# Kernel optimization log

Hardware: AMD Instinct MI355X
Metric: run time of the kernel (lower is better)

The kernel has to match this reference:

```python
import jax, jax.numpy as jnp
import numpy as np

NUM_NODES = 100000
EMB = 64
HID = 128
OUT = 64
N_EDGES = 1600000
N_LABEL = 200000


def setup_inputs() -> dict:
    key = jax.random.key(0)
    ks = jax.random.split(key, 8)
    return {
        "emb": jax.random.normal(ks[0], (NUM_NODES, EMB), jnp.float32) * 0.05,
        "w1l": jax.random.normal(ks[1], (HID, EMB), jnp.float32) * 0.05,
        "w1r": jax.random.normal(ks[2], (HID, EMB), jnp.float32) * 0.05,
        "b1": jnp.zeros((HID,), jnp.float32),
        "w2l": jax.random.normal(ks[3], (OUT, HID), jnp.float32) * 0.05,
        "w2r": jax.random.normal(ks[4], (OUT, HID), jnp.float32) * 0.05,
        "b2": jnp.zeros((OUT,), jnp.float32),
        "edge_index": jax.random.randint(ks[5], (2, N_EDGES), 0, NUM_NODES, jnp.int32),
        "edge_label_index": jax.random.randint(ks[6], (2, N_LABEL), 0, NUM_NODES, jnp.int32),
    }


def reference(emb, w1l, w1r, b1, w2l, w2r, b2, edge_index, edge_label_index):
    # PyG SAGEConv (aggr='mean'): out = mean_{j in N(i)} x_j @ W_l^T + b_l + x_i @ W_r^T
    n = emb.shape[0]
    src, dst = edge_index[0], edge_index[1]
    # in-degree per destination node, clamped to avoid div-by-zero (isolated nodes -> 0 agg)
    deg = jax.ops.segment_sum(jnp.ones(src.shape, emb.dtype), dst, num_segments=n)
    inv_deg = 1.0 / jnp.maximum(deg, 1.0)

    def sage(x, wl, wr, b):
        agg = jax.ops.segment_sum(x[src], dst, num_segments=n) * inv_deg[:, None]
        return agg @ wl.T + x @ wr.T + b

    h = jax.nn.relu(sage(emb, w1l, w1r, b1))  # dropout is identity in eval mode
    z = sage(h, w2l, w2r, b2)  # [N, OUT]
    # dot-product decode over candidate pairs
    return jnp.sum(z[edge_label_index[0]] * z[edge_label_index[1]], axis=-1)
```

## Files before the change

kernel.cpp:

```cpp
#include <hip/hip_runtime.h>

#define NN   100000
#define EMB  64
#define HID  128
#define OUTD 64
#define NE   1600000
#define NL   200000
#define NBUK 782
#define CAPT 2560

#define BIN_BLOCKS  160
#define TILE        10240
#define CEMB_BLOCKS 400
#define CW_BLOCKS   32

typedef __attribute__((ext_vector_type(4))) float f32x4;
typedef __attribute__((ext_vector_type(8))) short s16x8;
typedef __attribute__((ext_vector_type(4))) unsigned short us4;

__device__ __forceinline__ unsigned short f2bf(float f) {
    unsigned u = __float_as_uint(f);
    u += 0x7FFFu + ((u >> 16) & 1u);
    return (unsigned short)(u >> 16);
}
__device__ __forceinline__ float bf2f(unsigned short h) {
    return __uint_as_float(((unsigned)h) << 16);
}

__global__ void __launch_bounds__(512) prep_kernel(
        const int* __restrict__ src, const int* __restrict__ dst,
        int* __restrict__ gcur, int* __restrict__ tmp,
        const float* __restrict__ emb, unsigned short* __restrict__ embb,
        const float* __restrict__ w1l, const float* __restrict__ w1r,
        const float* __restrict__ w2l, const float* __restrict__ w2r,
        unsigned short* __restrict__ w1cat, unsigned short* __restrict__ w2cat) {
    const int bid = blockIdx.x;
    const int tid = threadIdx.x;

    if (bid < BIN_BLOCKS) {
        __shared__ int hist[NBUK];
        __shared__ int base[NBUK];
        const int t0  = bid * TILE;
        const int end = min(t0 + TILE, NE);

        for (int k = tid; k < NBUK; k += 512) hist[k] = 0;
        __syncthreads();

        for (int i = t0 + tid; i < end; i += 512)
            atomicAdd(&hist[__builtin_nontemporal_load(dst + i) >> 7], 1);
        __syncthreads();

        for (int k = tid; k < NBUK; k += 512) {
            int c = hist[k];
            base[k] = c ? atomicAdd(&gcur[k], c) : 0;
        }
        __syncthreads();

        for (int i = t0 + tid; i < end; i += 512) {
            int d = __builtin_nontemporal_load(dst + i);
            int s = __builtin_nontemporal_load(src + i);
            int b = d >> 7;
            int pos = atomicAdd(&base[b], 1);
            if (pos < CAPT) tmp[b * CAPT + pos] = ((d & 127) << 17) | s;
        }
    } else if (bid < BIN_BLOCKS + CEMB_BLOCKS) {
        for (int i = (bid - BIN_BLOCKS) * 512 + tid; i < NN * 16; i += CEMB_BLOCKS * 512) {
            float4 v = ((const float4*)emb)[i];
            us4 o;
            o.x = f2bf(v.x); o.y = f2bf(v.y); o.z = f2bf(v.z); o.w = f2bf(v.w);
            ((us4*)embb)[i] = o;
        }
    } else {
        int t = (bid - BIN_BLOCKS - CEMB_BLOCKS) * 512 + tid;
        if (t >= 128 * 128) return;
        int o = t >> 7, k = t & 127;
        w1cat[t] = f2bf(k < 64 ? w1l[o * 64 + k] : w1r[o * 64 + (k - 64)]);
        w2cat[t] = f2bf(o < 64 ? w2l[o * 128 + k] : w2r[(o - 64) * 128 + k]);
    }
}

template<bool L1>
__global__ void __launch_bounds__(512) agg_kernel(
        const int* __restrict__ gcur, const int* __restrict__ tmp,
        const unsigned short* __restrict__ xb,
        const float* __restrict__ hz, const float* __restrict__ bias,
        unsigned short* __restrict__ outb) {
    __shared__ int scnt[128];
    __shared__ int soff[128];
    __shared__ int scur[128];
    __shared__ int slist[CAPT];

    const int b    = blockIdx.x;
    const int tid  = threadIdx.x;
    const int lane = tid & 63;
    const int wv   = tid >> 6;

    if (tid < 128) scnt[tid] = 0;
    __syncthreads();

    const int cnt = min(gcur[b], CAPT);
    const int* tb = tmp + b * CAPT;

    for (int i = tid; i < cnt; i += 512)
        atomicAdd(&scnt[tb[i] >> 17], 1);
    __syncthreads();

    if (tid == 0) {
        int acc = 0;
        for (int r = 0; r < 128; ++r) {
            soff[r] = acc;
            scur[r] = acc;
            acc += scnt[r];
        }
    }
    __syncthreads();

    for (int i = tid; i < cnt; i += 512) {
        int p = tb[i];
        int pos = atomicAdd(&scur[p >> 17], 1);
        slist[pos] = p & 0x1FFFF;
    }
    __syncthreads();

    const float bb = L1 ? 0.f : bias[lane];

#define LDX(c) bf2f(xb[(size_t)(c) * 64 + lane])
    for (int r = wv; r < 128; r += 8) {
        const int node = b * 128 + r;
        if (node >= NN) continue;
        const int s = soff[r];
        const int d = scnt[r];
        float acc = 0.f;
        int j = 0;
        for (; j + 8 <= d; j += 8) {
            int c0 = slist[s + j + 0], c1 = slist[s + j + 1];
            int c2 = slist[s + j + 2], c3 = slist[s + j + 3];
            int c4 = slist[s + j + 4], c5 = slist[s + j + 5];
            int c6 = slist[s + j + 6], c7 = slist[s + j + 7];
            float v0 = LDX(c0), v1 = LDX(c1), v2 = LDX(c2), v3 = LDX(c3);
            float v4 = LDX(c4), v5 = LDX(c5), v6 = LDX(c6), v7 = LDX(c7);
            acc += ((v0 + v1) + (v2 + v3)) + ((v4 + v5) + (v6 + v7));
        }
        if (j + 4 <= d) {
            int c0 = slist[s + j + 0], c1 = slist[s + j + 1];
            int c2 = slist[s + j + 2], c3 = slist[s + j + 3];
            float v0 = LDX(c0), v1 = LDX(c1), v2 = LDX(c2), v3 = LDX(c3);
            acc += (v0 + v1) + (v2 + v3);
            j += 4;
        }
        for (; j < d; ++j) acc += LDX(slist[s + j]);

        const float inv = 1.0f / fmaxf((float)d, 1.0f);
        if (L1) {
            outb[(size_t)node * 64 + lane] = f2bf(acc * inv);
        } else {
            outb[(size_t)node * 64 + lane] =
                f2bf(acc * inv + hz[(size_t)node * 64 + lane] + bb);
        }
    }
#undef LDX
}

__global__ void __launch_bounds__(256) gemm_mfma_kernel(
        const unsigned short* __restrict__ aggb, const unsigned short* __restrict__ embb,
        const unsigned short* __restrict__ w1cat, const float* __restrict__ b1,
        const unsigned short* __restrict__ w2cat,
        unsigned short* __restrict__ p2b, float* __restrict__ hz) {
    __shared__ unsigned short h_lds[128 * 136];

    const int tid  = threadIdx.x;
    const int lane = tid & 63;
    const int w    = tid >> 6;
    const int l15  = lane & 15;
    const int lk   = lane >> 4;
    const int n_base = blockIdx.x * 128;
    const int mrow0  = w * 32;

    f32x4 acc[2][8];
#pragma unroll
    for (int mt = 0; mt < 2; ++mt)
#pragma unroll
        for (int nt = 0; nt < 8; ++nt) acc[mt][nt] = (f32x4)(0.f);

#pragma unroll
    for (int ks = 0; ks < 4; ++ks) {
        const int kc = ks * 32 + lk * 8;
        s16x8 a[2];
#pragma unroll
        for (int mt = 0; mt < 2; ++mt) {
            int n = n_base + mrow0 + mt * 16 + l15;
            s16x8 av = (s16x8)(short)0;
            if (n < NN) {
                const unsigned short* ap = (kc < 64)
                    ? (aggb + (size_t)n * 64 + kc)
                    : (embb + (size_t)n * 64 + (kc - 64));
                av = *(const s16x8*)ap;
            }
            a[mt] = av;
        }
#pragma unroll
        for (int nt = 0; nt < 8; ++nt) {
            s16x8 bv = *(const s16x8*)(w1cat + (nt * 16 + l15) * 128 + kc);
            acc[0][nt] = __builtin_amdgcn_mfma_f32_16x16x32_bf16(a[0], bv, acc[0][nt], 0, 0, 0);
            acc[1][nt] = __builtin_amdgcn_mfma_f32_16x16x32_bf16(a[1], bv, acc[1][nt], 0, 0, 0);
        }
    }

    float b1v[8];
#pragma unroll
    for (int nt = 0; nt < 8; ++nt) b1v[nt] = b1[nt * 16 + l15];
#pragma unroll
    for (int mt = 0; mt < 2; ++mt)
#pragma unroll
        for (int nt = 0; nt < 8; ++nt) {
            f32x4 d = acc[mt][nt];
            int o = nt * 16 + l15;
            int r0 = mrow0 + mt * 16 + lk * 4;
#pragma unroll
            for (int j = 0; j < 4; ++j)
                h_lds[(r0 + j) * 136 + o] = f2bf(fmaxf(d[j] + b1v[nt], 0.f));
        }

#pragma unroll
    for (int mt = 0; mt < 2; ++mt)
#pragma unroll
        for (int nt = 0; nt < 8; ++nt) acc[mt][nt] = (f32x4)(0.f);

#pragma unroll
    for (int ks = 0; ks < 4; ++ks) {
        const int kc = ks * 32 + lk * 8;
        s16x8 a[2];
#pragma unroll
        for (int mt = 0; mt < 2; ++mt)
            a[mt] = *(const s16x8*)&h_lds[(mrow0 + mt * 16 + l15) * 136 + kc];
#pragma unroll
        for (int nt = 0; nt < 8; ++nt) {
            s16x8 bv = *(const s16x8*)(w2cat + (nt * 16 + l15) * 128 + kc);
            acc[0][nt] = __builtin_amdgcn_mfma_f32_16x16x32_bf16(a[0], bv, acc[0][nt], 0, 0, 0);
            acc[1][nt] = __builtin_amdgcn_mfma_f32_16x16x32_bf16(a[1], bv, acc[1][nt], 0, 0, 0);
        }
    }

#pragma unroll
    for (int mt = 0; mt < 2; ++mt)
#pragma unroll
        for (int nt = 0; nt < 8; ++nt) {
            f32x4 d = acc[mt][nt];
            int o = nt * 16 + l15;
            int r0 = n_base + mrow0 + mt * 16 + lk * 4;
#pragma unroll
            for (int j = 0; j < 4; ++j) {
                int r = r0 + j;
                if (r >= NN) continue;
                if (nt < 4) p2b[(size_t)r * 64 + o] = f2bf(d[j]);
                else        hz[(size_t)r * 64 + (o - 64)] = d[j];
            }
        }
}

__global__ void decode_kernel(const int* __restrict__ a, const int* __restrict__ b,
                              const unsigned short* __restrict__ zb, float* __restrict__ out) {
    int t = blockIdx.x * blockDim.x + threadIdx.x;
    int k = t >> 4;
    int q = t & 15;
    if (k >= NL) return;
    int ia = a[k], ib = b[k];
    us4 va = ((const us4*)zb)[ia * 16 + q];
    us4 vb = ((const us4*)zb)[ib * 16 + q];
    float s = bf2f(va.x) * bf2f(vb.x) + bf2f(va.y) * bf2f(vb.y)
            + bf2f(va.z) * bf2f(vb.z) + bf2f(va.w) * bf2f(vb.w);
    s += __shfl_xor(s, 1, 64);
    s += __shfl_xor(s, 2, 64);
    s += __shfl_xor(s, 4, 64);
    s += __shfl_xor(s, 8, 64);
    if (q == 0) __builtin_nontemporal_store(s, out + k);
}

extern "C" void kernel_launch(void* const* d_in, const int* in_sizes, int n_in,
                              void* d_out, int out_size, void* d_ws, size_t ws_size,
                              hipStream_t stream) {
    const float* emb = (const float*)d_in[0];
    const float* w1l = (const float*)d_in[1];
    const float* w1r = (const float*)d_in[2];
    const float* b1  = (const float*)d_in[3];
    const float* w2l = (const float*)d_in[4];
    const float* w2r = (const float*)d_in[5];
    const float* b2  = (const float*)d_in[6];
    const int*   ei  = (const int*)d_in[7];
    const int*   eli = (const int*)d_in[8];
    float* out = (float*)d_out;

    int* gcur = (int*)d_ws;
    int* tmp  = gcur + 1024;
    unsigned short* aggb  = (unsigned short*)(tmp + (size_t)NBUK * CAPT);
    unsigned short* embb  = aggb + (size_t)NN * 64;
    unsigned short* p2b   = embb + (size_t)NN * 64;
    unsigned short* zb    = p2b + (size_t)NN * 64;
    unsigned short* w1cat = zb + (size_t)NN * 64;
    unsigned short* w2cat = w1cat + 128 * 128;
    float* hz = (float*)(w2cat + 128 * 128);

    const int* src = ei;
    const int* dst = ei + NE;

    hipMemsetAsync(gcur, 0, 1024 * sizeof(int), stream);

    prep_kernel<<<BIN_BLOCKS + CEMB_BLOCKS + CW_BLOCKS, 512, 0, stream>>>(
        src, dst, gcur, tmp, emb, embb, w1l, w1r, w2l, w2r, w1cat, w2cat);

    agg_kernel<true><<<NBUK, 512, 0, stream>>>(gcur, tmp, embb, nullptr, nullptr, aggb);

    const int NT = (NN + 127) / 128;
    gemm_mfma_kernel<<<NT, 256, 0, stream>>>(aggb, embb, w1cat, b1, w2cat, p2b, hz);

    agg_kernel<false><<<NBUK, 512, 0, stream>>>(gcur, tmp, p2b, hz, b2, zb);

    decode_kernel<<<(NL * 16 + 255) / 256, 256, 0, stream>>>(eli, eli + NL, zb, out);
}
```

Baseline: 198.9 us.

## Store hz in bf16, use 512-thread GEMM blocks, stage outputs through LDS

The x@W2r term (hz) is now written and read as bf16 instead of fp32, halving that intermediate's traffic in both the GEMM and the second aggregation kernel. The GEMM kernel goes to 512 threads, with each wave covering 16 rows instead of 32. This cuts accumulator registers per thread and A operands are preloaded up front. Outputs are staged through LDS so each lane writes 16-byte vectorized, coalesced rows instead of scattered 2- and 4-byte stores. Rounding hz to bf16 adds a small precision loss.

```diff
diff --git a/kernel.cpp b/kernel.cpp
--- a/kernel.cpp
+++ b/kernel.cpp
@@ -17,6 +17,7 @@
 typedef __attribute__((ext_vector_type(4))) float f32x4;
 typedef __attribute__((ext_vector_type(8))) short s16x8;
 typedef __attribute__((ext_vector_type(4))) unsigned short us4;
+typedef __attribute__((ext_vector_type(8))) unsigned short us8;
 
 __device__ __forceinline__ unsigned short f2bf(float f) {
     unsigned u = __float_as_uint(f);
@@ -83,7 +84,7 @@
 __global__ void __launch_bounds__(512) agg_kernel(
         const int* __restrict__ gcur, const int* __restrict__ tmp,
         const unsigned short* __restrict__ xb,
-        const float* __restrict__ hz, const float* __restrict__ bias,
+        const unsigned short* __restrict__ hzb, const float* __restrict__ bias,
         unsigned short* __restrict__ outb) {
     __shared__ int scnt[128];
     __shared__ int soff[128];
@@ -155,17 +156,17 @@
             outb[(size_t)node * 64 + lane] = f2bf(acc * inv);
         } else {
             outb[(size_t)node * 64 + lane] =
-                f2bf(acc * inv + hz[(size_t)node * 64 + lane] + bb);
+                f2bf(acc * inv + bf2f(hzb[(size_t)node * 64 + lane]) + bb);
         }
     }
 #undef LDX
 }
 
-__global__ void __launch_bounds__(256) gemm_mfma_kernel(
+__global__ void __launch_bounds__(512) gemm_mfma_kernel(
         const unsigned short* __restrict__ aggb, const unsigned short* __restrict__ embb,
         const unsigned short* __restrict__ w1cat, const float* __restrict__ b1,
         const unsigned short* __restrict__ w2cat,
-        unsigned short* __restrict__ p2b, float* __restrict__ hz) {
+        unsigned short* __restrict__ p2b, unsigned short* __restrict__ hzb) {
     __shared__ unsigned short h_lds[128 * 136];
 
     const int tid  = threadIdx.x;
@@ -174,35 +175,35 @@
     const int l15  = lane & 15;
     const int lk   = lane >> 4;
     const int n_base = blockIdx.x * 128;
-    const int mrow0  = w * 32;
-
-    f32x4 acc[2][8];
-#pragma unroll
-    for (int mt = 0; mt < 2; ++mt)
-#pragma unroll
-        for (int nt = 0; nt < 8; ++nt) acc[mt][nt] = (f32x4)(0.f);
-
-#pragma unroll
-    for (int ks = 0; ks < 4; ++ks) {
-        const int kc = ks * 32 + lk * 8;
-        s16x8 a[2];
-#pragma unroll
-        for (int mt = 0; mt < 2; ++mt) {
-            int n = n_base + mrow0 + mt * 16 + l15;
-            s16x8 av = (s16x8)(short)0;
-            if (n < NN) {
+    const int mrow0  = w * 16;
+
+    f32x4 acc[8];
+#pragma unroll
+    for (int nt = 0; nt < 8; ++nt) acc[nt] = (f32x4)(0.f);
+
+    s16x8 a[4];
+    {
+        const int n = n_base + mrow0 + l15;
+        const bool ok = n < NN;
+#pragma unroll
+        for (int ks = 0; ks < 4; ++ks) {
+            const int kc = ks * 32 + lk * 8;
+            a[ks] = (s16x8)(short)0;
+            if (ok) {
                 const unsigned short* ap = (kc < 64)
                     ? (aggb + (size_t)n * 64 + kc)
                     : (embb + (size_t)n * 64 + (kc - 64));
-                av = *(const s16x8*)ap;
+                a[ks] = *(const s16x8*)ap;
             }
-            a[mt] = av;
-        }
+        }
+    }
+#pragma unroll
+    for (int ks = 0; ks < 4; ++ks) {
+        const int kc = ks * 32 + lk * 8;
 #pragma unroll
         for (int nt = 0; nt < 8; ++nt) {
             s16x8 bv = *(const s16x8*)(w1cat + (nt * 16 + l15) * 128 + kc);
-            acc[0][nt] = __builtin_amdgcn_mfma_f32_16x16x32_bf16(a[0], bv, acc[0][nt], 0, 0, 0);
-            acc[1][nt] = __builtin_amdgcn_mfma_f32_16x16x32_bf16(a[1], bv, acc[1][nt], 0, 0, 0);
+            acc[nt] = __builtin_amdgcn_mfma_f32_16x16x32_bf16(a[ks], bv, acc[nt], 0, 0, 0);
         }
     }
 
@@ -210,52 +211,56 @@
 #pragma unroll
     for (int nt = 0; nt < 8; ++nt) b1v[nt] = b1[nt * 16 + l15];
 #pragma unroll
-    for (int mt = 0; mt < 2; ++mt)
-#pragma unroll
-        for (int nt = 0; nt < 8; ++nt) {
-            f32x4 d = acc[mt][nt];
-            int o = nt * 16 + l15;
-            int r0 = mrow0 + mt * 16 + lk * 4;
-#pragma unroll
-            for (int j = 0; j < 4; ++j)
-                h_lds[(r0 + j) * 136 + o] = f2bf(fmaxf(d[j] + b1v[nt], 0.f));
-        }
-
-#pragma unroll
-    for (int mt = 0; mt < 2; ++mt)
-#pragma unroll
-        for (int nt = 0; nt < 8; ++nt) acc[mt][nt] = (f32x4)(0.f);
-
+    for (int nt = 0; nt < 8; ++nt) {
+        f32x4 d = acc[nt];
+        int o = nt * 16 + l15;
+        int r0 = mrow0 + lk * 4;
+#pragma unroll
+        for (int j = 0; j < 4; ++j)
+            h_lds[(r0 + j) * 136 + o] = f2bf(fmaxf(d[j] + b1v[nt], 0.f));
+    }
+
+#pragma unroll
+    for (int nt = 0; nt < 8; ++nt) acc[nt] = (f32x4)(0.f);
+
+    s16x8 a2[4];
+#pragma unroll
+    for (int ks = 0; ks < 4; ++ks)
+        a2[ks] = *(const s16x8*)&h_lds[(mrow0 + l15) * 136 + ks * 32 + lk * 8];
 #pragma unroll
     for (int ks = 0; ks < 4; ++ks) {
         const int kc = ks * 32 + lk * 8;
-        s16x8 a[2];
-#pragma unroll
-        for (int mt = 0; mt < 2; ++mt)
-            a[mt] = *(const s16x8*)&h_lds[(mrow0 + mt * 16 + l15) * 136 + kc];
 #pragma unroll
         for (int nt = 0; nt < 8; ++nt) {
             s16x8 bv = *(const s16x8*)(w2cat + (nt * 16 + l15) * 128 + kc);
-            acc[0][nt] = __builtin_amdgcn_mfma_f32_16x16x32_bf16(a[0], bv, acc[0][nt], 0, 0, 0);
-            acc[1][nt] = __builtin_amdgcn_mfma_f32_16x16x32_bf16(a[1], bv, acc[1][nt], 0, 0, 0);
-        }
-    }
-
-#pragma unroll
-    for (int mt = 0; mt < 2; ++mt)
-#pragma unroll
-        for (int nt = 0; nt < 8; ++nt) {
-            f32x4 d = acc[mt][nt];
-            int o = nt * 16 + l15;
-            int r0 = n_base + mrow0 + mt * 16 + lk * 4;
-#pragma unroll
-            for (int j = 0; j < 4; ++j) {
-                int r = r0 + j;
-                if (r >= NN) continue;
-                if (nt < 4) p2b[(size_t)r * 64 + o] = f2bf(d[j]);
-                else        hz[(size_t)r * 64 + (o - 64)] = d[j];
+            acc[nt] = __builtin_amdgcn_mfma_f32_16x16x32_bf16(a2[ks], bv, acc[nt], 0, 0, 0);
+        }
+    }
+
+#pragma unroll
+    for (int nt = 0; nt < 8; ++nt) {
+        f32x4 d = acc[nt];
+        int col = nt * 16 + l15;
+        int r0 = mrow0 + lk * 4;
+#pragma unroll
+        for (int j = 0; j < 4; ++j)
+            h_lds[(r0 + j) * 136 + col] = f2bf(d[j]);
+    }
+    {
+        const int row8 = lane >> 3;
+        const int seg  = lane & 7;
+#pragma unroll
+        for (int half = 0; half < 2; ++half) {
+            int r = mrow0 + half * 8 + row8;
+            int n = n_base + r;
+            us8 vp = *(const us8*)&h_lds[r * 136 + seg * 8];
+            us8 vh = *(const us8*)&h_lds[r * 136 + 64 + seg * 8];
+            if (n < NN) {
+                *(us8*)&p2b[(size_t)n * 64 + seg * 8] = vp;
+                *(us8*)&hzb[(size_t)n * 64 + seg * 8] = vh;
             }
         }
+    }
 }
 
 __global__ void decode_kernel(const int* __restrict__ a, const int* __restrict__ b,
@@ -296,9 +301,9 @@
     unsigned short* embb  = aggb + (size_t)NN * 64;
     unsigned short* p2b   = embb + (size_t)NN * 64;
     unsigned short* zb    = p2b + (size_t)NN * 64;
-    unsigned short* w1cat = zb + (size_t)NN * 64;
+    unsigned short* hzb   = zb + (size_t)NN * 64;
+    unsigned short* w1cat = hzb + (size_t)NN * 64;
     unsigned short* w2cat = w1cat + 128 * 128;
-    float* hz = (float*)(w2cat + 128 * 128);
 
     const int* src = ei;
     const int* dst = ei + NE;
@@ -311,9 +316,9 @@
     agg_kernel<true><<<NBUK, 512, 0, stream>>>(gcur, tmp, embb, nullptr, nullptr, aggb);
 
     const int NT = (NN + 127) / 128;
-    gemm_mfma_kernel<<<NT, 256, 0, stream>>>(aggb, embb, w1cat, b1, w2cat, p2b, hz);
-
-    agg_kernel<false><<<NBUK, 512, 0, stream>>>(gcur, tmp, p2b, hz, b2, zb);
+    gemm_mfma_kernel<<<NT, 512, 0, stream>>>(aggb, embb, w1cat, b1, w2cat, p2b, hzb);
+
+    agg_kernel<false><<<NBUK, 512, 0, stream>>>(gcur, tmp, p2b, hzb, b2, zb);
 
     decode_kernel<<<(NL * 16 + 255) / 256, 256, 0, stream>>>(eli, eli + NL, zb, out);
 }
```

Measured after the change: 216.8 us. +9.0%, slower.
